# Kernel optimization log

Measured on AMD Instinct MI355X. Metric: run time of the kernel, lower is better.

Reference implementation:

```python
import jax, jax.numpy as jnp
import numpy as np
import math

C_S, C_Z = 384, 128
N_HEAD, C = 12, 16
N_QP, N_PV = 4, 8
B, N_RES = 1, 384


def quat_to_rot(q):
    # q: (..., 4) unnormalized quaternion -> (..., 3, 3) rotation matrix
    q = q / jnp.linalg.norm(q, axis=-1, keepdims=True)
    w, x, y, z = q[..., 0], q[..., 1], q[..., 2], q[..., 3]
    R = jnp.stack([
        1 - 2 * (y * y + z * z), 2 * (x * y - w * z), 2 * (x * z + w * y),
        2 * (x * y + w * z), 1 - 2 * (x * x + z * z), 2 * (y * z - w * x),
        2 * (x * z - w * y), 2 * (y * z + w * x), 1 - 2 * (x * x + y * y),
    ], axis=-1)
    return R.reshape(q.shape[:-1] + (3, 3))


def warp_3d_point(T, p):
    # T: (..., 1, 1, N, 4, 4) rigid transforms; p: (..., H, P, N, 3)
    R = T[..., :3, :3]
    t = T[..., :3, 3]
    return jnp.squeeze(R @ p[..., None], -1) + t


def warp_3d_point_inv(T, p):
    # Inverse rigid transform: R^T (p - t)
    R = T[..., :3, :3]
    t = T[..., :3, 3]
    return jnp.squeeze(jnp.swapaxes(R, -1, -2) @ (p - t)[..., None], -1)


def setup_inputs() -> dict:
    key = jax.random.key(0)
    ks = jax.random.split(key, 24)
    s = jax.random.normal(ks[0], (B, N_RES, C_S), dtype=jnp.float32)
    z = jax.random.normal(ks[1], (B, N_RES, N_RES, C_Z), dtype=jnp.float32)
    # Build rigid backbone transforms T (rotation from random quaternion + translation)
    quat = jax.random.normal(ks[2], (B, N_RES, 4), dtype=jnp.float32)
    trans = jax.random.normal(ks[3], (B, N_RES, 3), dtype=jnp.float32) * 10.0
    R = quat_to_rot(quat)
    T = jnp.zeros((B, N_RES, 4, 4), dtype=jnp.float32)
    T = T.at[..., :3, :3].set(R)
    T = T.at[..., :3, 3].set(trans)
    T = T.at[..., 3, 3].set(1.0)

    def lin(k, din, dout):
        kw, kb = jax.random.split(k)
        W = jax.random.normal(kw, (din, dout), dtype=jnp.float32) * 0.02
        b = jax.random.normal(kb, (dout,), dtype=jnp.float32) * 0.01
        return W, b

    Wq, bq = lin(ks[4], C_S, N_HEAD * C)
    Wk, bk = lin(ks[5], C_S, N_HEAD * C)
    Wv, bv = lin(ks[6], C_S, N_HEAD * C)
    Wqp, bqp = lin(ks[7], C_S, 3 * N_QP * N_HEAD)
    Wkp, bkp = lin(ks[8], C_S, 3 * N_QP * N_HEAD)
    Wvp, bvp = lin(ks[9], C_S, 3 * N_PV * N_HEAD)
    Wb, bb = lin(ks[10], C_Z, N_HEAD)
    d_out_in = N_HEAD * C_Z + N_HEAD * C + N_HEAD * 4 * N_PV
    Wo, bo = lin(ks[11], d_out_in, C_S)
    head_weights = jax.random.normal(ks[12], (N_HEAD,), dtype=jnp.float32) * 0.1
    return dict(s=s, z=z, T=T, Wq=Wq, bq=bq, Wk=Wk, bk=bk, Wv=Wv, bv=bv,
                Wqp=Wqp, bqp=bqp, Wkp=Wkp, bkp=bkp, Wvp=Wvp, bvp=bvp,
                Wb=Wb, bb=bb, Wo=Wo, bo=bo, head_weights=head_weights)


def ipa_forward(s, z, T, Wq, bq, Wk, bk, Wv, bv, Wqp, bqp, Wkp, bkp,
                Wvp, bvp, Wb, bb, Wo, bo, head_weights):
    batch = s.shape[:-2]
    n = s.shape[-2]
    # --- prepare qkv ---
    def heads(x):  # (..., N, H*C) -> (..., H, N, C)
        return jnp.moveaxis(x.reshape(batch + (n, N_HEAD, C)), -3, -2)
    q = heads(s @ Wq + bq)
    k = heads(s @ Wk + bk)
    v = heads(s @ Wv + bv)

    def pts(x, P):  # (..., N, 3*H*P) -> (..., H, P, N, 3)
        x = x.reshape(batch + (n, 3, N_HEAD, P))
        return jnp.moveaxis(x, (-4, -3), (-2, -1))
    qp = pts(s @ Wqp + bqp, N_QP)
    kp = pts(s @ Wkp + bkp, N_QP)
    vp = pts(s @ Wvp + bvp, N_PV)

    # --- attention scores (Alg 22 line 7) ---
    wc = math.sqrt(2.0 / (9.0 * N_QP))
    wl = math.sqrt(1.0 / 3.0)
    gamma = jax.nn.softplus(head_weights).reshape(-1, 1, 1)  # (H,1,1)
    q = q * (1.0 / math.sqrt(C))
    bias = jnp.moveaxis(z @ Wb + bb, -1, -3)  # (..., H, N, N)
    qk = jnp.einsum('...hic,...hjc->...hij', q, k)
    T_bc = T.reshape(batch + (1, 1, n, 4, 4))
    tqp = warp_3d_point(T_bc, qp)[..., :, None, :]   # (..., H, QP, N, 1, 3)
    tkp = warp_3d_point(T_bc, kp)[..., None, :, :]   # (..., H, QP, 1, N, 3)
    sq_dist = jnp.sum((tqp - tkp) ** 2, axis=-1)      # (..., H, QP, N, N)
    qpkp_term = gamma * (wc / 2.0) * jnp.sum(sq_dist, axis=-3)  # (..., H, N, N)
    att = jax.nn.softmax(wl * (qk + bias - qpkp_term), axis=-1)

    # --- outputs ---
    pairwise = jnp.einsum('...ijc,...hij->...hic', z, att)
    pairwise = jnp.moveaxis(pairwise, -3, -2).reshape(batch + (n, N_HEAD * C_Z))
    v_out = jnp.einsum('...hij,...hjc->...hic', att, v)
    v_out = jnp.moveaxis(v_out, -3, -2).reshape(batch + (n, N_HEAD * C))
    vt = warp_3d_point(T_bc, vp)                                # (..., H, PV, N, 3)
    v_att = jnp.einsum('...hij,...hkjp->...hkip', att, vt)     # (..., H, PV, N, 3)
    v_tr = warp_3d_point_inv(T_bc, v_att)                       # (..., H, PV, N, 3)
    v_tr = jnp.einsum('...hpic->...ichp', v_tr)                 # (..., N, 3, H, PV)
    norm = jnp.linalg.norm(v_tr, axis=-3, keepdims=True)        # (..., N, 1, H, PV)
    vp_norm = norm.reshape(batch + (n, N_HEAD * N_PV))
    vp_out = v_tr.reshape(batch + (n, 3 * N_HEAD * N_PV))

    out = jnp.concatenate([v_out, vp_out, vp_norm, pairwise], axis=-1)
    return out @ Wo + bo


def reference(s, z, T, Wq, bq, Wk, bk, Wv, bv, Wqp, bqp, Wkp, bkp,
              Wvp, bvp, Wb, bb, Wo, bo, head_weights):
    return ipa_forward(s, z, T, Wq, bq, Wk, bk, Wv, bv, Wqp, bqp, Wkp, bkp,
                       Wvp, bvp, Wb, bb, Wo, bo, head_weights)
```

## Files before the change

kernel.cpp:

```cpp
#include <hip/hip_runtime.h>
#include <math.h>

#define NRES 384
#define NH   12
#define WLc 0.5773502691896258f
#define WCc 0.23570226039551587f

typedef __attribute__((ext_vector_type(8))) _Float16 half8;
typedef __attribute__((ext_vector_type(4))) float f32x4;

#define OFF_P    0
#define OFF_PW   0
#define OFF_SH   442368
#define OFF_WCT  516096
#define OFF_BCT  737280
#define OFF_QE   738432
#define OFF_KE   885888
#define OFF_VET  1033344
#define OFF_WOT  1143936
#define OFF_CAT  1549440
#define OFF_ATT  1954944
#define OFF_BIAS 2839680
#define OFF_Z16  3724416

__global__ __launch_bounds__(256) void pack_bias(
    const float* __restrict__ s,  const float* __restrict__ z,
    const float* __restrict__ Wq,  const float* __restrict__ bq,
    const float* __restrict__ Wk,  const float* __restrict__ bk,
    const float* __restrict__ Wv,  const float* __restrict__ bv,
    const float* __restrict__ Wqp, const float* __restrict__ bqp,
    const float* __restrict__ Wkp, const float* __restrict__ bkp,
    const float* __restrict__ Wvp, const float* __restrict__ bvp,
    const float* __restrict__ Wb,  const float* __restrict__ bb,
    const float* __restrict__ Wo,
    float* __restrict__ ws)
{
    int b = blockIdx.x, t = threadIdx.x;
    __shared__ float tile[64 * 65];
    __shared__ _Float16 wbT[16 * 136];
    __shared__ float sbb[16];
    __shared__ _Float16 zL[64 * 136];

    if (b >= 451) {
        _Float16* biasb = (_Float16*)(ws + OFF_BIAS);
        _Float16* z16t  = (_Float16*)(ws + OFF_Z16);
        int bi = b - 451;
        size_t m0 = (size_t)bi * 64;
        int ib = bi / 6, j0 = (bi % 6) * 64;
        if (t < 128) {
            #pragma unroll
            for (int h = 0; h < 12; h++) wbT[h * 136 + t] = (_Float16)(WLc * Wb[t * 12 + h]);
            #pragma unroll
            for (int h = 12; h < 16; h++) wbT[h * 136 + t] = (_Float16)0.f;
        }
        if (t < 16) sbb[t] = (t < 12) ? WLc * bb[t] : 0.f;
        __syncthreads();
        int w = t >> 6, lane = t & 63;
        int m = lane & 15, q = lane >> 4;
        size_t ri = m0 + w * 16 + m;
        const float* zr = z + ri * 128 + q * 8;
        f32x4 acc = {0};
        #pragma unroll
        for (int sI = 0; sI < 4; sI++) {
            float4 v0 = *(const float4*)(zr + sI * 32);
            float4 v1 = *(const float4*)(zr + sI * 32 + 4);
            half8 a;
            a[0]=(_Float16)v0.x; a[1]=(_Float16)v0.y; a[2]=(_Float16)v0.z; a[3]=(_Float16)v0.w;
            a[4]=(_Float16)v1.x; a[5]=(_Float16)v1.y; a[6]=(_Float16)v1.z; a[7]=(_Float16)v1.w;
            *(half8*)(zL + (w * 16 + m) * 136 + sI * 32 + q * 8) = a;
            half8 bf = *(const half8*)(wbT + m * 136 + sI * 32 + q * 8);
            acc = __builtin_amdgcn_mfma_f32_16x16x32_f16(a, bf, acc, 0, 0, 0);
        }
        __syncthreads();
        {
            int c = t & 127, jh = t >> 7;
            _Float16 vals[32];
            #pragma unroll
            for (int u = 0; u < 32; u++) vals[u] = zL[(jh * 32 + u) * 136 + c];
            _Float16* dst = z16t + ((size_t)ib * 128 + c) * 384 + j0 + jh * 32;
            #pragma unroll
            for (int g = 0; g < 4; g++) {
                half8 r;
                #pragma unroll
                for (int u = 0; u < 8; u++) r[u] = vals[g * 8 + u];
                *(half8*)(dst + g * 8) = r;
            }
        }
        if (m < 12) {
            #pragma unroll
            for (int r = 0; r < 4; r++)
                biasb[(size_t)m * 147456 + m0 + w * 16 + q * 4 + r] = (_Float16)(acc[r] + sbb[m]);
        }
        return;
    }

    _Float16* sh  = (_Float16*)(ws + OFF_SH);
    _Float16* wct = (_Float16*)(ws + OFF_WCT);
    _Float16* wot = (_Float16*)(ws + OFF_WOT);
    float* bct = ws + OFF_BCT;

    if (b < 144) {
        int id = b * 256 + t;
        float4 v = ((const float4*)s)[id];
        _Float16 r[4] = { (_Float16)v.x, (_Float16)v.y, (_Float16)v.z, (_Float16)v.w };
        *(uint2*)(sh + id * 4) = *(uint2*)r;
        return;
    }
    if (b < 252) {
        int ti = b - 144;
        int k0 = (ti % 6) * 64, n0 = (ti / 6) * 64;
        int cl = t & 63, rg = t >> 6;
        int ncat = n0 + cl;
        const float* W; int dout, col;
        if      (ncat < 192) { W = Wq;  dout = 192; col = ncat; }
        else if (ncat < 384) { W = Wk;  dout = 192; col = ncat - 192; }
        else if (ncat < 576) { W = Wv;  dout = 192; col = ncat - 384; }
        else if (ncat < 720) { W = Wqp; dout = 144; col = ncat - 576; }
        else if (ncat < 864) { W = Wkp; dout = 144; col = ncat - 720; }
        else                 { W = Wvp; dout = 288; col = ncat - 864; }
        #pragma unroll
        for (int u = 0; u < 16; u++) {
            int r = rg * 16 + u;
            tile[r * 65 + cl] = W[(size_t)(k0 + r) * dout + col];
        }
        __syncthreads();
        #pragma unroll
        for (int u2 = 0; u2 < 2; u2++) {
            int item = t + 256 * u2;
            int nl = item >> 3, kg = item & 7;
            half8 rr;
            #pragma unroll
            for (int jj = 0; jj < 8; jj++) rr[jj] = (_Float16)tile[(kg * 8 + jj) * 65 + nl];
            *(half8*)(wct + (size_t)(n0 + nl) * 384 + k0 + kg * 8) = rr;
        }
        return;
    }
    if (b < 450) {
        int ti = b - 252;
        int k0 = (ti % 33) * 64, n0 = (ti / 33) * 64;
        int cl = t & 63, rg = t >> 6;
        #pragma unroll
        for (int u = 0; u < 16; u++) {
            int r = rg * 16 + u;
            tile[r * 65 + cl] = Wo[(size_t)(k0 + r) * 384 + n0 + cl];
        }
        __syncthreads();
        #pragma unroll
        for (int u2 = 0; u2 < 2; u2++) {
            int item = t + 256 * u2;
            int nl = item >> 3, kg = item & 7;
            half8 rr;
            #pragma unroll
            for (int jj = 0; jj < 8; jj++) rr[jj] = (_Float16)tile[(kg * 8 + jj) * 65 + nl];
            *(half8*)(wot + (size_t)(n0 + nl) * 2112 + k0 + kg * 8) = rr;
        }
        return;
    }
    for (int e = t; e < 1152; e += 256) {
        float bv_;
        if      (e < 192) bv_ = bq[e];
        else if (e < 384) bv_ = bk[e - 192];
        else if (e < 576) bv_ = bv[e - 384];
        else if (e < 720) bv_ = bqp[e - 576];
        else if (e < 864) bv_ = bkp[e - 720];
        else              bv_ = bvp[e - 864];
        bct[e] = bv_;
    }
}

__global__ __launch_bounds__(256) void proj_mfma(float* __restrict__ ws)
{
    const _Float16* sh  = (const _Float16*)(ws + OFF_SH);
    const _Float16* wct = (const _Float16*)(ws + OFF_WCT);
    const float* bct = ws + OFF_BCT;
    float* P = ws + OFF_P;

    __shared__ float sAcc[2][16][65];

    int t = threadIdx.x, w = t >> 6, lane = t & 63;
    int m = lane & 15, q = lane >> 4;
    int mh = w & 1, kh = w >> 1;
    int n0 = blockIdx.x * 64, m0 = blockIdx.y * 32 + mh * 16;

    f32x4 acc[4] = {0};
    const _Float16* arow = sh + (size_t)(m0 + m) * 384 + kh * 192;
    #pragma unroll 3
    for (int s = 0; s < 6; s++) {
        int k = s * 32 + q * 8;
        half8 a = *(const half8*)(arow + k);
        #pragma unroll
        for (int nt = 0; nt < 4; nt++) {
            half8 b = *(const half8*)(wct + (size_t)(n0 + nt * 16 + m) * 384 + kh * 192 + k);
            acc[nt] = __builtin_amdgcn_mfma_f32_16x16x32_f16(a, b, acc[nt], 0, 0, 0);
        }
    }
    if (kh == 0) {
        #pragma unroll
        for (int nt = 0; nt < 4; nt++)
            #pragma unroll
            for (int r = 0; r < 4; r++)
                sAcc[mh][q * 4 + r][nt * 16 + m] = acc[nt][r];
    }
    __syncthreads();
    if (kh == 1) {
        #pragma unroll
        for (int nt = 0; nt < 4; nt++) {
            int col = n0 + nt * 16 + m;
            float bias = bct[col];
            #pragma unroll
            for (int r = 0; r < 4; r++)
                P[(size_t)(m0 + q * 4 + r) * 1152 + col] =
                    acc[nt][r] + sAcc[mh][q * 4 + r][nt * 16 + m] + bias;
        }
    }
}

__global__ __launch_bounds__(192) void prep_kernel(
    const float* __restrict__ T, const float* __restrict__ hw,
    const float* __restrict__ bo, float* __restrict__ out,
    float* __restrict__ ws)
{
    int i = blockIdx.x, t = threadIdx.x;
    const float* pr = ws + OFF_P + (size_t)i * 1152;
    float* Qe = ws + OFF_QE;
    float* Ke = ws + OFF_KE;
    _Float16* vet = (_Float16*)(ws + OFF_VET);

    out[(size_t)i * 384 + t]       = bo[t];
    out[(size_t)i * 384 + 192 + t] = bo[192 + t];

    __shared__ float sT[16], sG[12];
    __shared__ float sTQ[12][4][3], sTK[12][4][3];
    if (t < 16) sT[t] = T[i * 16 + t];
    if (t < 12) { float x = hw[t]; sG[t] = (x > 20.f) ? x : log1pf(__expf(x)); }
    __syncthreads();
    float R00=sT[0],R01=sT[1],R02=sT[2],t0=sT[3];
    float R10=sT[4],R11=sT[5],R12=sT[6],t1=sT[7];
    float R20=sT[8],R21=sT[9],R22=sT[10],t2=sT[11];

    if (t < 48) {
        int h = t >> 2, p = t & 3;
        float a0 = pr[576 + 0*48 + h*4 + p], a1 = pr[576 + 1*48 + h*4 + p], a2 = pr[576 + 2*48 + h*4 + p];
        sTQ[h][p][0] = R00*a0 + R01*a1 + R02*a2 + t0;
        sTQ[h][p][1] = R10*a0 + R11*a1 + R12*a2 + t1;
        sTQ[h][p][2] = R20*a0 + R21*a1 + R22*a2 + t2;
    } else if (t < 96) {
        int tt = t - 48, h = tt >> 2, p = tt & 3;
        float a0 = pr[720 + 0*48 + h*4 + p], a1 = pr[720 + 1*48 + h*4 + p], a2 = pr[720 + 2*48 + h*4 + p];
        sTK[h][p][0] = R00*a0 + R01*a1 + R02*a2 + t0;
        sTK[h][p][1] = R10*a0 + R11*a1 + R12*a2 + t1;
        sTK[h][p][2] = R20*a0 + R21*a1 + R22*a2 + t2;
    } else {
        int tt = t - 96, h = tt >> 3, p = tt & 7;
        float a0 = pr[864 + 0*96 + h*8 + p], a1 = pr[864 + 1*96 + h*8 + p], a2 = pr[864 + 2*96 + h*8 + p];
        vet[(size_t)(h*48 + 16 + p*3 + 0) * 384 + i] = (_Float16)(R00*a0 + R01*a1 + R02*a2 + t0);
        vet[(size_t)(h*48 + 16 + p*3 + 1) * 384 + i] = (_Float16)(R10*a0 + R11*a1 + R12*a2 + t1);
        vet[(size_t)(h*48 + 16 + p*3 + 2) * 384 + i] = (_Float16)(R20*a0 + R21*a1 + R22*a2 + t2);
    }
    {
        int h = t >> 4, c = t & 15;
        vet[(size_t)(h*48 + c) * 384 + i] = (_Float16)pr[384 + h*16 + c];
        if (t < 96) vet[(size_t)((t>>3)*48 + 40 + (t&7)) * 384 + i] = (_Float16)0.f;
        Qe[(size_t)i*384 + h*32 + c] = WLc * 0.25f * pr[h*16 + c];
        Ke[((size_t)h*384 + i)*32 + c] = pr[192 + h*16 + c];
    }
    __syncthreads();
    if (t < 144) {
        int h = t / 12, d = t % 12, p = d / 3, r = d % 3;
        float gw = WLc * sG[h] * WCc;
        Qe[(size_t)i*384 + h*32 + 16 + d] = gw * sTQ[h][p][r];
        Ke[((size_t)h*384 + i)*32 + 16 + d] = sTK[h][p][r];
    }
    if (t < 12) {
        int h = t;
        float sqq = 0.f, sqk = 0.f;
        #pragma unroll
        for (int p = 0; p < 4; p++)
            #pragma unroll
            for (int r = 0; r < 3; r++) { sqq += sTQ[h][p][r]*sTQ[h][p][r]; sqk += sTK[h][p][r]*sTK[h][p][r]; }
        float gw = WLc * sG[h] * WCc;
        Qe[(size_t)i*384 + h*32 + 28] = -0.5f * gw;
        Qe[(size_t)i*384 + h*32 + 29] = -0.5f * gw * sqq;
        Qe[(size_t)i*384 + h*32 + 30] = 0.f;
        Qe[(size_t)i*384 + h*32 + 31] = 0.f;
        Ke[((size_t)h*384 + i)*32 + 28] = sqk;
        Ke[((size_t)h*384 + i)*32 + 29] = 1.f;
        Ke[((size_t)h*384 + i)*32 + 30] = 0.f;
        Ke[((size_t)h*384 + i)*32 + 31] = 0.f;
    }
}

__global__ __launch_bounds__(512) void logits_out40(
    const float* __restrict__ T, float* __restrict__ ws)
{
    __shared__ float sQe[8 * 32];
    __shared__ float sLg[8][384];
    __shared__ float sMS[16];
    __shared__ _Float16 sAttL[8 * 392];
    __shared__ float sO[8 * 49];
    __shared__ float sT8[8 * 16];

    int h = blockIdx.y, i0 = blockIdx.x * 8;
    int t = threadIdx.x;
    const float* Qe = ws + OFF_QE;
    const float* Ke = ws + OFF_KE;
    const _Float16* biasb = (const _Float16*)(ws + OFF_BIAS);
    const _Float16* vet = (const _Float16*)(ws + OFF_VET);
    _Float16* attg = (_Float16*)(ws + OFF_ATT);
    _Float16* catb = (_Float16*)(ws + OFF_CAT);

    {
        int bid = blockIdx.y * 48 + blockIdx.x;
        if (t < 256)
            ((float4*)(ws + OFF_PW))[bid * 256 + t] = (float4){0.f, 0.f, 0.f, 0.f};
    }
    if (t < 256)
        sQe[t] = Qe[(size_t)(i0 + (t >> 5)) * 384 + h * 32 + (t & 31)];
    if (t < 128)
        sT8[t] = T[(size_t)(i0 + (t >> 4)) * 16 + (t & 15)];
    __syncthreads();

    float lgv[8];
    if (t < 384) {
        int j = t;
        float ke[32];
        const float4* kr = (const float4*)(Ke + ((size_t)h * 384 + j) * 32);
        #pragma unroll
        for (int u = 0; u < 8; u++) { float4 v = kr[u]; ke[u*4]=v.x; ke[u*4+1]=v.y; ke[u*4+2]=v.z; ke[u*4+3]=v.w; }
        #pragma unroll
        for (int ii = 0; ii < 8; ii++) {
            float acc = (float)biasb[(size_t)h * 147456 + (size_t)(i0 + ii) * 384 + j];
            #pragma unroll
            for (int c = 0; c < 32; c++) acc += sQe[ii * 32 + c] * ke[c];
            lgv[ii] = acc;
            sLg[ii][j] = acc;
        }
    }
    __syncthreads();
    {
        int w = t >> 6, lane = t & 63;
        float vv[6], mx = -1e30f;
        #pragma unroll
        for (int u = 0; u < 6; u++) { vv[u] = sLg[w][lane + 64 * u]; mx = fmaxf(mx, vv[u]); }
        #pragma unroll
        for (int off = 1; off < 64; off <<= 1) mx = fmaxf(mx, __shfl_xor(mx, off));
        float sm = 0.f;
        #pragma unroll
        for (int u = 0; u < 6; u++) sm += __expf(vv[u] - mx);
        #pragma unroll
        for (int off = 1; off < 64; off <<= 1) sm += __shfl_xor(sm, off);
        if (lane == 0) { sMS[w] = mx; sMS[8 + w] = sm; }
    }
    __syncthreads();
    if (t < 384) {
        int j = t;
        #pragma unroll
        for (int ii = 0; ii < 8; ii++) {
            float a = __expf(lgv[ii] - sMS[ii]) * (1.0f / sMS[8 + ii]);
            attg[((size_t)h * 384 + i0 + ii) * 384 + j] = (_Float16)a;
            sAttL[ii * 392 + j] = (_Float16)a;
        }
    }
    __syncthreads();

    int w = t >> 6, lane = t & 63;
    int m16 = lane & 15, q = lane >> 4;
    if (w < 3) {
        int nt = w;
        f32x4 acc = {0};
        #pragma unroll 3
        for (int s = 0; s < 12; s++) {
            int k = s * 32 + q * 8;
            half8 a;
            if (m16 < 8) a = *(const half8*)(sAttL + m16 * 392 + k);
            else         a = (half8){0,0,0,0,0,0,0,0};
            half8 bfr = *(const half8*)(vet + (size_t)(h * 48 + nt * 16 + m16) * 384 + k);
            acc = __builtin_amdgcn_mfma_f32_16x16x32_f16(a, bfr, acc, 0, 0, 0);
        }
        #pragma unroll
        for (int r = 0; r < 4; r++) {
            int row = q * 4 + r;
            if (row < 8) sO[row * 49 + nt * 16 + m16] = acc[r];
        }
    }
    __syncthreads();

    if (t < 128) {
        int il = t >> 4, c = t & 15;
        catb[(size_t)(i0 + il) * 576 + h * 16 + c] = (_Float16)sO[il * 49 + c];
    }
    if (t < 64) {
        int il = t >> 3, p = t & 7;
        const float* o = sO + il * 49 + 16 + p * 3;
        const float* Ti = sT8 + il * 16;
        float x0 = o[0] - Ti[3], x1 = o[1] - Ti[7], x2 = o[2] - Ti[11];
        float r0 = Ti[0]*x0 + Ti[4]*x1 + Ti[8]*x2;
        float r1 = Ti[1]*x0 + Ti[5]*x1 + Ti[9]*x2;
        float r2 = Ti[2]*x0 + Ti[6]*x1 + Ti[10]*x2;
        _Float16* cr = catb + (size_t)(i0 + il) * 576;
        cr[192 + 0*96 + h*8 + p] = (_Float16)r0;
        cr[192 + 1*96 + h*8 + p] = (_Float16)r1;
        cr[192 + 2*96 + h*8 + p] = (_Float16)r2;
        cr[480 + h*8 + p] = (_Float16)sqrtf(r0*r0 + r1*r1 + r2*r2);
    }
}

__global__ __launch_bounds__(256) void pairwise_mfma(float* __restrict__ ws)
{
    int i = blockIdx.x, jc = blockIdx.y;
    int t = threadIdx.x, w = t >> 6, lane = t & 63;
    int m16 = lane & 15, q = lane >> 4;
    const _Float16* attg = (const _Float16*)(ws + OFF_ATT);
    const _Float16* z16t = (const _Float16*)(ws + OFF_Z16);
    float* PW = ws + OFF_PW;

    f32x4 acc0 = {0}, acc1 = {0};
    const _Float16* arow  = attg + ((size_t)(m16 < 12 ? m16 : 0) * 384 + i) * 384 + jc * 128;
    const _Float16* zrow0 = z16t + ((size_t)i * 128 + w * 32 + m16) * 384 + jc * 128;
    const _Float16* zrow1 = zrow0 + 16 * 384;
    #pragma unroll
    for (int ks = 0; ks < 4; ks++) {
        int k = ks * 32 + q * 8;
        half8 a;
        if (m16 < 12) a = *(const half8*)(arow + k);
        else          a = (half8){0,0,0,0,0,0,0,0};
        half8 b0 = *(const half8*)(zrow0 + k);
        half8 b1 = *(const half8*)(zrow1 + k);
        acc0 = __builtin_amdgcn_mfma_f32_16x16x32_f16(a, b0, acc0, 0, 0, 0);
        acc1 = __builtin_amdgcn_mfma_f32_16x16x32_f16(a, b1, acc1, 0, 0, 0);
    }
    if (q < 3) {
        #pragma unroll
        for (int r = 0; r < 4; r++) {
            int h = q * 4 + r;
            atomicAdd(&PW[(size_t)i * 1536 + h * 128 + w * 32 + m16],      acc0[r]);
            atomicAdd(&PW[(size_t)i * 1536 + h * 128 + w * 32 + 16 + m16], acc1[r]);
        }
    }
}

__global__ __launch_bounds__(256) void outgemm_mfma(
    float* __restrict__ ws, float* __restrict__ out)
{
    const _Float16* catb = (const _Float16*)(ws + OFF_CAT);
    const float* PW = ws + OFF_PW;
    const _Float16* wot = (const _Float16*)(ws + OFF_WOT);

    __shared__ float sAcc[2][16][65];

    int t = threadIdx.x, w = t >> 6, lane = t & 63;
    int m = lane & 15, q = lane >> 4;
    int mh = w & 1, kh = w >> 1;
    int n0 = blockIdx.x * 64;
    int m0 = blockIdx.y * 32 + mh * 16;
    int kbase = blockIdx.z * 704 + kh * 352;

    f32x4 acc[4] = {0};
    int row = m0 + m;
    #pragma unroll 2
    for (int s = 0; s < 11; s++) {
        int kb = kbase + s * 32;
        int k = kb + q * 8;
        half8 a;
        if (kb < 576) {
            a = *(const half8*)(catb + (size_t)row * 576 + k);
        } else {
            const float* pwp = PW + (size_t)row * 1536 + (k - 576);
            float4 u0 = ((const float4*)pwp)[0];
            float4 u1 = ((const float4*)pwp)[1];
            a[0]=(_Float16)u0.x; a[1]=(_Float16)u0.y; a[2]=(_Float16)u0.z; a[3]=(_Float16)u0.w;
            a[4]=(_Float16)u1.x; a[5]=(_Float16)u1.y; a[6]=(_Float16)u1.z; a[7]=(_Float16)u1.w;
        }
        #pragma unroll
        for (int nt = 0; nt < 4; nt++) {
            half8 b = *(const half8*)(wot + (size_t)(n0 + nt * 16 + m) * 2112 + k);
            acc[nt] = __builtin_amdgcn_mfma_f32_16x16x32_f16(a, b, acc[nt], 0, 0, 0);
        }
    }
    if (kh == 0) {
        #pragma unroll
        for (int nt = 0; nt < 4; nt++)
            #pragma unroll
            for (int r = 0; r < 4; r++)
                sAcc[mh][q * 4 + r][nt * 16 + m] = acc[nt][r];
    }
    __syncthreads();
    if (kh == 1) {
        #pragma unroll
        for (int nt = 0; nt < 4; nt++) {
            int col = n0 + nt * 16 + m;
            #pragma unroll
            for (int r = 0; r < 4; r++)
                atomicAdd(&out[(size_t)(m0 + q * 4 + r) * 384 + col],
                          acc[nt][r] + sAcc[mh][q * 4 + r][nt * 16 + m]);
        }
    }
}

extern "C" void kernel_launch(void* const* d_in, const int* in_sizes, int n_in,
                              void* d_out, int out_size, void* d_ws, size_t ws_size,
                              hipStream_t stream)
{
    const float* s   = (const float*)d_in[0];
    const float* z   = (const float*)d_in[1];
    const float* T   = (const float*)d_in[2];
    const float* Wq  = (const float*)d_in[3];
    const float* bq  = (const float*)d_in[4];
    const float* Wk  = (const float*)d_in[5];
    const float* bk  = (const float*)d_in[6];
    const float* Wv  = (const float*)d_in[7];
    const float* bv  = (const float*)d_in[8];
    const float* Wqp = (const float*)d_in[9];
    const float* bqp = (const float*)d_in[10];
    const float* Wkp = (const float*)d_in[11];
    const float* bkp = (const float*)d_in[12];
    const float* Wvp = (const float*)d_in[13];
    const float* bvp = (const float*)d_in[14];
    const float* Wb  = (const float*)d_in[15];
    const float* bb  = (const float*)d_in[16];
    const float* Wo  = (const float*)d_in[17];
    const float* bo  = (const float*)d_in[18];
    const float* hw  = (const float*)d_in[19];
    float* ws  = (float*)d_ws;
    float* out = (float*)d_out;

    pack_bias<<<2755, 256, 0, stream>>>(s, z, Wq, bq, Wk, bk, Wv, bv,
                                        Wqp, bqp, Wkp, bkp, Wvp, bvp, Wb, bb, Wo, ws);
    proj_mfma<<<dim3(18, 12), 256, 0, stream>>>(ws);
    prep_kernel<<<384, 192, 0, stream>>>(T, hw, bo, out, ws);
    logits_out40<<<dim3(48, 12), 512, 0, stream>>>(T, ws);
    pairwise_mfma<<<dim3(384, 3), 256, 0, stream>>>(ws);
    outgemm_mfma<<<dim3(6, 12, 3), 256, 0, stream>>>(ws, out);
}
```

Measured before the change: 216.8 us.

## Fuse all IPA stages into one persistent cooperative kernel with grid syncs

Replaces the six separate kernel launches with a single cooperative persistent kernel that loops over each stage's work items and separates stages with grid-wide barriers. The aim is to remove per-launch overhead and the idle tail between dependent kernels. The old launch sequence stays as a fallback if the cooperative launch fails. In exchange, the logits stage now runs with 256 threads instead of 512. Grid syncs across up to 2048 blocks have their own cost, and shared memory is a single union buffer sized for the largest stage.

```diff
diff --git a/kernel.cpp b/kernel.cpp
--- a/kernel.cpp
+++ b/kernel.cpp
@@ -1,5 +1,8 @@
 #include <hip/hip_runtime.h>
+#include <hip/hip_cooperative_groups.h>
 #include <math.h>
+
+namespace cg = cooperative_groups;
 
 #define NRES 384
 #define NH   12
@@ -22,6 +25,489 @@
 #define OFF_ATT  1954944
 #define OFF_BIAS 2839680
 #define OFF_Z16  3724416
+
+__global__ __launch_bounds__(256, 3) void mega_ipa(
+    const float* __restrict__ s,  const float* __restrict__ z,
+    const float* __restrict__ T,  const float* __restrict__ hw,
+    const float* __restrict__ Wq,  const float* __restrict__ bq,
+    const float* __restrict__ Wk,  const float* __restrict__ bk,
+    const float* __restrict__ Wv,  const float* __restrict__ bv,
+    const float* __restrict__ Wqp, const float* __restrict__ bqp,
+    const float* __restrict__ Wkp, const float* __restrict__ bkp,
+    const float* __restrict__ Wvp, const float* __restrict__ bvp,
+    const float* __restrict__ Wb,  const float* __restrict__ bb,
+    const float* __restrict__ Wo,  const float* __restrict__ bo,
+    float* __restrict__ ws, float* __restrict__ out)
+{
+    cg::grid_group grid = cg::this_grid();
+    __shared__ __attribute__((aligned(16))) char smem[21888];
+
+    const int t = threadIdx.x;
+    const int bid = blockIdx.x;
+    const int G = gridDim.x;
+    const int w = t >> 6, lane = t & 63;
+    const int m16 = lane & 15, q4 = lane >> 4;
+
+    {
+        float* tile    = (float*)smem;
+        _Float16* zL   = (_Float16*)smem;
+        _Float16* wbT  = (_Float16*)(smem + 17408);
+        float* sbb     = (float*)(smem + 21760);
+        _Float16* sh   = (_Float16*)(ws + OFF_SH);
+        _Float16* wct  = (_Float16*)(ws + OFF_WCT);
+        _Float16* wot  = (_Float16*)(ws + OFF_WOT);
+        float* bct     = ws + OFF_BCT;
+        _Float16* biasb = (_Float16*)(ws + OFF_BIAS);
+        _Float16* z16t  = (_Float16*)(ws + OFF_Z16);
+
+        for (int b = bid; b < 2755; b += G) {
+            if (b >= 451) {
+                int bi = b - 451;
+                size_t m0 = (size_t)bi * 64;
+                int ib = bi / 6, j0 = (bi % 6) * 64;
+                if (t < 128) {
+                    #pragma unroll
+                    for (int h = 0; h < 12; h++) wbT[h * 136 + t] = (_Float16)(WLc * Wb[t * 12 + h]);
+                    #pragma unroll
+                    for (int h = 12; h < 16; h++) wbT[h * 136 + t] = (_Float16)0.f;
+                }
+                if (t < 16) sbb[t] = (t < 12) ? WLc * bb[t] : 0.f;
+                __syncthreads();
+                size_t ri = m0 + w * 16 + m16;
+                const float* zr = z + ri * 128 + q4 * 8;
+                f32x4 acc = {0};
+                #pragma unroll
+                for (int sI = 0; sI < 4; sI++) {
+                    float4 v0 = *(const float4*)(zr + sI * 32);
+                    float4 v1 = *(const float4*)(zr + sI * 32 + 4);
+                    half8 a;
+                    a[0]=(_Float16)v0.x; a[1]=(_Float16)v0.y; a[2]=(_Float16)v0.z; a[3]=(_Float16)v0.w;
+                    a[4]=(_Float16)v1.x; a[5]=(_Float16)v1.y; a[6]=(_Float16)v1.z; a[7]=(_Float16)v1.w;
+                    *(half8*)(zL + (w * 16 + m16) * 136 + sI * 32 + q4 * 8) = a;
+                    half8 bf = *(const half8*)(wbT + m16 * 136 + sI * 32 + q4 * 8);
+                    acc = __builtin_amdgcn_mfma_f32_16x16x32_f16(a, bf, acc, 0, 0, 0);
+                }
+                __syncthreads();
+                {
+                    int c = t & 127, jh = t >> 7;
+                    _Float16 vals[32];
+                    #pragma unroll
+                    for (int u = 0; u < 32; u++) vals[u] = zL[(jh * 32 + u) * 136 + c];
+                    _Float16* dst = z16t + ((size_t)ib * 128 + c) * 384 + j0 + jh * 32;
+                    #pragma unroll
+                    for (int g = 0; g < 4; g++) {
+                        half8 r;
+                        #pragma unroll
+                        for (int u = 0; u < 8; u++) r[u] = vals[g * 8 + u];
+                        *(half8*)(dst + g * 8) = r;
+                    }
+                }
+                if (m16 < 12) {
+                    #pragma unroll
+                    for (int r = 0; r < 4; r++)
+                        biasb[(size_t)m16 * 147456 + m0 + w * 16 + q4 * 4 + r] = (_Float16)(acc[r] + sbb[m16]);
+                }
+            } else if (b < 144) {
+                int id = b * 256 + t;
+                float4 v = ((const float4*)s)[id];
+                _Float16 r[4] = { (_Float16)v.x, (_Float16)v.y, (_Float16)v.z, (_Float16)v.w };
+                *(uint2*)(sh + id * 4) = *(uint2*)r;
+            } else if (b < 252) {
+                int ti = b - 144;
+                int k0 = (ti % 6) * 64, n0 = (ti / 6) * 64;
+                int cl = t & 63, rg = t >> 6;
+                int ncat = n0 + cl;
+                const float* W; int dout, col;
+                if      (ncat < 192) { W = Wq;  dout = 192; col = ncat; }
+                else if (ncat < 384) { W = Wk;  dout = 192; col = ncat - 192; }
+                else if (ncat < 576) { W = Wv;  dout = 192; col = ncat - 384; }
+                else if (ncat < 720) { W = Wqp; dout = 144; col = ncat - 576; }
+                else if (ncat < 864) { W = Wkp; dout = 144; col = ncat - 720; }
+                else                 { W = Wvp; dout = 288; col = ncat - 864; }
+                #pragma unroll
+                for (int u = 0; u < 16; u++) {
+                    int r = rg * 16 + u;
+                    tile[r * 65 + cl] = W[(size_t)(k0 + r) * dout + col];
+                }
+                __syncthreads();
+                #pragma unroll
+                for (int u2 = 0; u2 < 2; u2++) {
+                    int item = t + 256 * u2;
+                    int nl = item >> 3, kg = item & 7;
+                    half8 rr;
+                    #pragma unroll
+                    for (int jj = 0; jj < 8; jj++) rr[jj] = (_Float16)tile[(kg * 8 + jj) * 65 + nl];
+                    *(half8*)(wct + (size_t)(n0 + nl) * 384 + k0 + kg * 8) = rr;
+                }
+            } else if (b < 450) {
+                int ti = b - 252;
+                int k0 = (ti % 33) * 64, n0 = (ti / 33) * 64;
+                int cl = t & 63, rg = t >> 6;
+                #pragma unroll
+                for (int u = 0; u < 16; u++) {
+                    int r = rg * 16 + u;
+                    tile[r * 65 + cl] = Wo[(size_t)(k0 + r) * 384 + n0 + cl];
+                }
+                __syncthreads();
+                #pragma unroll
+                for (int u2 = 0; u2 < 2; u2++) {
+                    int item = t + 256 * u2;
+                    int nl = item >> 3, kg = item & 7;
+                    half8 rr;
+                    #pragma unroll
+                    for (int jj = 0; jj < 8; jj++) rr[jj] = (_Float16)tile[(kg * 8 + jj) * 65 + nl];
+                    *(half8*)(wot + (size_t)(n0 + nl) * 2112 + k0 + kg * 8) = rr;
+                }
+            } else {
+                for (int e = t; e < 1152; e += 256) {
+                    float bv_;
+                    if      (e < 192) bv_ = bq[e];
+                    else if (e < 384) bv_ = bk[e - 192];
+                    else if (e < 576) bv_ = bv[e - 384];
+                    else if (e < 720) bv_ = bqp[e - 576];
+                    else if (e < 864) bv_ = bkp[e - 720];
+                    else              bv_ = bvp[e - 864];
+                    bct[e] = bv_;
+                }
+            }
+            __syncthreads();
+        }
+    }
+    grid.sync();
+
+    {
+        const _Float16* sh  = (const _Float16*)(ws + OFF_SH);
+        const _Float16* wct = (const _Float16*)(ws + OFF_WCT);
+        const float* bct = ws + OFF_BCT;
+        float* P = ws + OFF_P;
+        float* sAcc = (float*)smem;
+        int mh = w & 1, kh = w >> 1;
+
+        for (int b = bid; b < 216; b += G) {
+            int n0 = (b % 18) * 64, m0 = (b / 18) * 32 + mh * 16;
+            f32x4 acc[4] = {0};
+            const _Float16* arow = sh + (size_t)(m0 + m16) * 384 + kh * 192;
+            #pragma unroll 3
+            for (int ss = 0; ss < 6; ss++) {
+                int k = ss * 32 + q4 * 8;
+                half8 a = *(const half8*)(arow + k);
+                #pragma unroll
+                for (int nt = 0; nt < 4; nt++) {
+                    half8 bfr = *(const half8*)(wct + (size_t)(n0 + nt * 16 + m16) * 384 + kh * 192 + k);
+                    acc[nt] = __builtin_amdgcn_mfma_f32_16x16x32_f16(a, bfr, acc[nt], 0, 0, 0);
+                }
+            }
+            if (kh == 0) {
+                #pragma unroll
+                for (int nt = 0; nt < 4; nt++)
+                    #pragma unroll
+                    for (int r = 0; r < 4; r++)
+                        sAcc[(mh * 16 + q4 * 4 + r) * 65 + nt * 16 + m16] = acc[nt][r];
+            }
+            __syncthreads();
+            if (kh == 1) {
+                #pragma unroll
+                for (int nt = 0; nt < 4; nt++) {
+                    int col = n0 + nt * 16 + m16;
+                    float bias = bct[col];
+                    #pragma unroll
+                    for (int r = 0; r < 4; r++)
+                        P[(size_t)(m0 + q4 * 4 + r) * 1152 + col] =
+                            acc[nt][r] + sAcc[(mh * 16 + q4 * 4 + r) * 65 + nt * 16 + m16] + bias;
+                }
+            }
+            __syncthreads();
+        }
+    }
+    grid.sync();
+
+    {
+        float* sT  = (float*)smem;
+        float* sG  = (float*)(smem + 64);
+        float* sTQ = (float*)(smem + 128);
+        float* sTK = (float*)(smem + 704);
+        float* Qe = ws + OFF_QE;
+        float* Ke = ws + OFF_KE;
+        _Float16* vet = (_Float16*)(ws + OFF_VET);
+
+        for (int b = bid; b < 384; b += G) {
+            int i = b;
+            const float* pr = ws + OFF_P + (size_t)i * 1152;
+            if (t < 192) {
+                out[(size_t)i * 384 + t]       = bo[t];
+                out[(size_t)i * 384 + 192 + t] = bo[192 + t];
+            }
+            if (t < 16) sT[t] = T[i * 16 + t];
+            if (t < 12) { float x = hw[t]; sG[t] = (x > 20.f) ? x : log1pf(__expf(x)); }
+            __syncthreads();
+            float R00=sT[0],R01=sT[1],R02=sT[2],t0=sT[3];
+            float R10=sT[4],R11=sT[5],R12=sT[6],t1=sT[7];
+            float R20=sT[8],R21=sT[9],R22=sT[10],t2=sT[11];
+
+            if (t < 48) {
+                int h = t >> 2, p = t & 3;
+                float a0 = pr[576 + 0*48 + h*4 + p], a1 = pr[576 + 1*48 + h*4 + p], a2 = pr[576 + 2*48 + h*4 + p];
+                sTQ[(h*4+p)*3+0] = R00*a0 + R01*a1 + R02*a2 + t0;
+                sTQ[(h*4+p)*3+1] = R10*a0 + R11*a1 + R12*a2 + t1;
+                sTQ[(h*4+p)*3+2] = R20*a0 + R21*a1 + R22*a2 + t2;
+            } else if (t < 96) {
+                int tt = t - 48, h = tt >> 2, p = tt & 3;
+                float a0 = pr[720 + 0*48 + h*4 + p], a1 = pr[720 + 1*48 + h*4 + p], a2 = pr[720 + 2*48 + h*4 + p];
+                sTK[(h*4+p)*3+0] = R00*a0 + R01*a1 + R02*a2 + t0;
+                sTK[(h*4+p)*3+1] = R10*a0 + R11*a1 + R12*a2 + t1;
+                sTK[(h*4+p)*3+2] = R20*a0 + R21*a1 + R22*a2 + t2;
+            } else if (t < 192) {
+                int tt = t - 96, h = tt >> 3, p = tt & 7;
+                float a0 = pr[864 + 0*96 + h*8 + p], a1 = pr[864 + 1*96 + h*8 + p], a2 = pr[864 + 2*96 + h*8 + p];
+                vet[(size_t)(h*48 + 16 + p*3 + 0) * 384 + i] = (_Float16)(R00*a0 + R01*a1 + R02*a2 + t0);
+                vet[(size_t)(h*48 + 16 + p*3 + 1) * 384 + i] = (_Float16)(R10*a0 + R11*a1 + R12*a2 + t1);
+                vet[(size_t)(h*48 + 16 + p*3 + 2) * 384 + i] = (_Float16)(R20*a0 + R21*a1 + R22*a2 + t2);
+            }
+            if (t < 192) {
+                int h = t >> 4, c = t & 15;
+                vet[(size_t)(h*48 + c) * 384 + i] = (_Float16)pr[384 + h*16 + c];
+                if (t < 96) vet[(size_t)((t>>3)*48 + 40 + (t&7)) * 384 + i] = (_Float16)0.f;
+                Qe[(size_t)i*384 + h*32 + c] = WLc * 0.25f * pr[h*16 + c];
+                Ke[((size_t)h*384 + i)*32 + c] = pr[192 + h*16 + c];
+            }
+            __syncthreads();
+            if (t < 144) {
+                int h = t / 12, d = t % 12, p = d / 3, r = d % 3;
+                float gw = WLc * sG[h] * WCc;
+                Qe[(size_t)i*384 + h*32 + 16 + d] = gw * sTQ[(h*4+p)*3+r];
+                Ke[((size_t)h*384 + i)*32 + 16 + d] = sTK[(h*4+p)*3+r];
+            }
+            if (t < 12) {
+                int h = t;
+                float sqq = 0.f, sqk = 0.f;
+                #pragma unroll
+                for (int p = 0; p < 4; p++)
+                    #pragma unroll
+                    for (int r = 0; r < 3; r++) {
+                        sqq += sTQ[(h*4+p)*3+r]*sTQ[(h*4+p)*3+r];
+                        sqk += sTK[(h*4+p)*3+r]*sTK[(h*4+p)*3+r];
+                    }
+                float gw = WLc * sG[h] * WCc;
+                Qe[(size_t)i*384 + h*32 + 28] = -0.5f * gw;
+                Qe[(size_t)i*384 + h*32 + 29] = -0.5f * gw * sqq;
+                Qe[(size_t)i*384 + h*32 + 30] = 0.f;
+                Qe[(size_t)i*384 + h*32 + 31] = 0.f;
+                Ke[((size_t)h*384 + i)*32 + 28] = sqk;
+                Ke[((size_t)h*384 + i)*32 + 29] = 1.f;
+                Ke[((size_t)h*384 + i)*32 + 30] = 0.f;
+                Ke[((size_t)h*384 + i)*32 + 31] = 0.f;
+            }
+            __syncthreads();
+        }
+    }
+    grid.sync();
+
+    {
+        float* sQe = (float*)smem;
+        float* sLg = (float*)(smem + 1024);
+        float* sMS = (float*)(smem + 13312);
+        _Float16* sAttL = (_Float16*)(smem + 13376);
+        float* sO  = (float*)(smem + 19648);
+        float* sT8 = (float*)(smem + 21216);
+        const float* Qe = ws + OFF_QE;
+        const float* Ke = ws + OFF_KE;
+        const _Float16* biasb = (const _Float16*)(ws + OFF_BIAS);
+        const _Float16* vet = (const _Float16*)(ws + OFF_VET);
+        _Float16* attg = (_Float16*)(ws + OFF_ATT);
+        _Float16* catb = (_Float16*)(ws + OFF_CAT);
+
+        for (int b = bid; b < 576; b += G) {
+            int h = b / 48, i0 = (b % 48) * 8;
+            ((float4*)(ws + OFF_PW))[b * 256 + t] = (float4){0.f, 0.f, 0.f, 0.f};
+            sQe[t] = Qe[(size_t)(i0 + (t >> 5)) * 384 + h * 32 + (t & 31)];
+            if (t < 128) sT8[t] = T[(size_t)(i0 + (t >> 4)) * 16 + (t & 15)];
+            __syncthreads();
+
+            float lgv[2][8];
+            if (t < 192) {
+                #pragma unroll
+                for (int jj = 0; jj < 2; jj++) {
+                    int j = t + jj * 192;
+                    float ke[32];
+                    const float4* kr = (const float4*)(Ke + ((size_t)h * 384 + j) * 32);
+                    #pragma unroll
+                    for (int u = 0; u < 8; u++) {
+                        float4 v = kr[u];
+                        ke[u*4]=v.x; ke[u*4+1]=v.y; ke[u*4+2]=v.z; ke[u*4+3]=v.w;
+                    }
+                    #pragma unroll
+                    for (int ii = 0; ii < 8; ii++) {
+                        float acc = (float)biasb[(size_t)h * 147456 + (size_t)(i0 + ii) * 384 + j];
+                        #pragma unroll
+                        for (int c = 0; c < 32; c++) acc += sQe[ii * 32 + c] * ke[c];
+                        lgv[jj][ii] = acc;
+                        sLg[ii * 384 + j] = acc;
+                    }
+                }
+            }
+            __syncthreads();
+            {
+                #pragma unroll
+                for (int rr = 0; rr < 2; rr++) {
+                    int row = w * 2 + rr;
+                    float vv[6], mx = -1e30f;
+                    #pragma unroll
+                    for (int u = 0; u < 6; u++) { vv[u] = sLg[row * 384 + lane + 64 * u]; mx = fmaxf(mx, vv[u]); }
+                    #pragma unroll
+                    for (int off = 1; off < 64; off <<= 1) mx = fmaxf(mx, __shfl_xor(mx, off));
+                    float sm = 0.f;
+                    #pragma unroll
+                    for (int u = 0; u < 6; u++) sm += __expf(vv[u] - mx);
+                    #pragma unroll
+                    for (int off = 1; off < 64; off <<= 1) sm += __shfl_xor(sm, off);
+                    if (lane == 0) { sMS[row] = mx; sMS[8 + row] = sm; }
+                }
+            }
+            __syncthreads();
+            if (t < 192) {
+                #pragma unroll
+                for (int jj = 0; jj < 2; jj++) {
+                    int j = t + jj * 192;
+                    #pragma unroll
+                    for (int ii = 0; ii < 8; ii++) {
+                        float a = __expf(lgv[jj][ii] - sMS[ii]) * (1.0f / sMS[8 + ii]);
+                        attg[((size_t)h * 384 + i0 + ii) * 384 + j] = (_Float16)a;
+                        sAttL[ii * 392 + j] = (_Float16)a;
+                    }
+                }
+            }
+            __syncthreads();
+            if (w < 3) {
+                int nt = w;
+                f32x4 acc = {0};
+                #pragma unroll 3
+                for (int ss = 0; ss < 12; ss++) {
+                    int k = ss * 32 + q4 * 8;
+                    half8 a;
+                    if (m16 < 8) a = *(const half8*)(sAttL + m16 * 392 + k);
+                    else         a = (half8){0,0,0,0,0,0,0,0};
+                    half8 bfr = *(const half8*)(vet + (size_t)(h * 48 + nt * 16 + m16) * 384 + k);
+                    acc = __builtin_amdgcn_mfma_f32_16x16x32_f16(a, bfr, acc, 0, 0, 0);
+                }
+                #pragma unroll
+                for (int r = 0; r < 4; r++) {
+                    int row = q4 * 4 + r;
+                    if (row < 8) sO[row * 49 + nt * 16 + m16] = acc[r];
+                }
+            }
+            __syncthreads();
+            if (t < 128) {
+                int il = t >> 4, c = t & 15;
+                catb[(size_t)(i0 + il) * 576 + h * 16 + c] = (_Float16)sO[il * 49 + c];
+            }
+            if (t < 64) {
+                int il = t >> 3, p = t & 7;
+                const float* o = sO + il * 49 + 16 + p * 3;
+                const float* Ti = sT8 + il * 16;
+                float x0 = o[0] - Ti[3], x1 = o[1] - Ti[7], x2 = o[2] - Ti[11];
+                float r0 = Ti[0]*x0 + Ti[4]*x1 + Ti[8]*x2;
+                float r1 = Ti[1]*x0 + Ti[5]*x1 + Ti[9]*x2;
+                float r2 = Ti[2]*x0 + Ti[6]*x1 + Ti[10]*x2;
+                _Float16* cr = catb + (size_t)(i0 + il) * 576;
+                cr[192 + 0*96 + h*8 + p] = (_Float16)r0;
+                cr[192 + 1*96 + h*8 + p] = (_Float16)r1;
+                cr[192 + 2*96 + h*8 + p] = (_Float16)r2;
+                cr[480 + h*8 + p] = (_Float16)sqrtf(r0*r0 + r1*r1 + r2*r2);
+            }
+            __syncthreads();
+        }
+    }
+    grid.sync();
+
+    {
+        const _Float16* attg = (const _Float16*)(ws + OFF_ATT);
+        const _Float16* z16t = (const _Float16*)(ws + OFF_Z16);
+        float* PW = ws + OFF_PW;
+
+        for (int b = bid; b < 1152; b += G) {
+            int i = b % 384, jc = b / 384;
+            f32x4 acc0 = {0}, acc1 = {0};
+            const _Float16* arow  = attg + ((size_t)(m16 < 12 ? m16 : 0) * 384 + i) * 384 + jc * 128;
+            const _Float16* zrow0 = z16t + ((size_t)i * 128 + w * 32 + m16) * 384 + jc * 128;
+            const _Float16* zrow1 = zrow0 + 16 * 384;
+            #pragma unroll
+            for (int ks = 0; ks < 4; ks++) {
+                int k = ks * 32 + q4 * 8;
+                half8 a;
+                if (m16 < 12) a = *(const half8*)(arow + k);
+                else          a = (half8){0,0,0,0,0,0,0,0};
+                half8 b0 = *(const half8*)(zrow0 + k);
+                half8 b1 = *(const half8*)(zrow1 + k);
+                acc0 = __builtin_amdgcn_mfma_f32_16x16x32_f16(a, b0, acc0, 0, 0, 0);
+                acc1 = __builtin_amdgcn_mfma_f32_16x16x32_f16(a, b1, acc1, 0, 0, 0);
+            }
+            if (q4 < 3) {
+                #pragma unroll
+                for (int r = 0; r < 4; r++) {
+                    int h = q4 * 4 + r;
+                    atomicAdd(&PW[(size_t)i * 1536 + h * 128 + w * 32 + m16],      acc0[r]);
+                    atomicAdd(&PW[(size_t)i * 1536 + h * 128 + w * 32 + 16 + m16], acc1[r]);
+                }
+            }
+        }
+    }
+    grid.sync();
+
+    {
+        const _Float16* catb = (const _Float16*)(ws + OFF_CAT);
+        const float* PW = ws + OFF_PW;
+        const _Float16* wot = (const _Float16*)(ws + OFF_WOT);
+        float* sAcc = (float*)smem;
+        int mh = w & 1, kh = w >> 1;
+
+        for (int b = bid; b < 216; b += G) {
+            int n0 = (b % 6) * 64;
+            int m0 = ((b / 6) % 12) * 32 + mh * 16;
+            int kbase = (b / 72) * 704 + kh * 352;
+            f32x4 acc[4] = {0};
+            int row = m0 + m16;
+            #pragma unroll 2
+            for (int ss = 0; ss < 11; ss++) {
+                int kb = kbase + ss * 32;
+                int k = kb + q4 * 8;
+                half8 a;
+                if (kb < 576) {
+                    a = *(const half8*)(catb + (size_t)row * 576 + k);
+                } else {
+                    const float* pwp = PW + (size_t)row * 1536 + (k - 576);
+                    float4 u0 = ((const float4*)pwp)[0];
+                    float4 u1 = ((const float4*)pwp)[1];
+                    a[0]=(_Float16)u0.x; a[1]=(_Float16)u0.y; a[2]=(_Float16)u0.z; a[3]=(_Float16)u0.w;
+                    a[4]=(_Float16)u1.x; a[5]=(_Float16)u1.y; a[6]=(_Float16)u1.z; a[7]=(_Float16)u1.w;
+                }
+                #pragma unroll
+                for (int nt = 0; nt < 4; nt++) {
+                    half8 bfr = *(const half8*)(wot + (size_t)(n0 + nt * 16 + m16) * 2112 + k);
+                    acc[nt] = __builtin_amdgcn_mfma_f32_16x16x32_f16(a, bfr, acc[nt], 0, 0, 0);
+                }
+            }
+            if (kh == 0) {
+                #pragma unroll
+                for (int nt = 0; nt < 4; nt++)
+                    #pragma unroll
+                    for (int r = 0; r < 4; r++)
+                        sAcc[(mh * 16 + q4 * 4 + r) * 65 + nt * 16 + m16] = acc[nt][r];
+            }
+            __syncthreads();
+            if (kh == 1) {
+                #pragma unroll
+                for (int nt = 0; nt < 4; nt++) {
+                    int col = n0 + nt * 16 + m16;
+                    #pragma unroll
+                    for (int r = 0; r < 4; r++)
+                        atomicAdd(&out[(size_t)(m0 + q4 * 4 + r) * 384 + col],
+                                  acc[nt][r] + sAcc[(mh * 16 + q4 * 4 + r) * 65 + nt * 16 + m16]);
+                }
+            }
+            __syncthreads();
+        }
+    }
+}
 
 __global__ __launch_bounds__(256) void pack_bias(
     const float* __restrict__ s,  const float* __restrict__ z,
@@ -174,14 +660,11 @@
     const _Float16* wct = (const _Float16*)(ws + OFF_WCT);
     const float* bct = ws + OFF_BCT;
     float* P = ws + OFF_P;
-
     __shared__ float sAcc[2][16][65];
-
     int t = threadIdx.x, w = t >> 6, lane = t & 63;
     int m = lane & 15, q = lane >> 4;
     int mh = w & 1, kh = w >> 1;
     int n0 = blockIdx.x * 64, m0 = blockIdx.y * 32 + mh * 16;
-
     f32x4 acc[4] = {0};
     const _Float16* arow = sh + (size_t)(m0 + m) * 384 + kh * 192;
     #pragma unroll 3
@@ -445,16 +928,13 @@
     const _Float16* catb = (const _Float16*)(ws + OFF_CAT);
     const float* PW = ws + OFF_PW;
     const _Float16* wot = (const _Float16*)(ws + OFF_WOT);
-
     __shared__ float sAcc[2][16][65];
-
     int t = threadIdx.x, w = t >> 6, lane = t & 63;
     int m = lane & 15, q = lane >> 4;
     int mh = w & 1, kh = w >> 1;
     int n0 = blockIdx.x * 64;
     int m0 = blockIdx.y * 32 + mh * 16;
     int kbase = blockIdx.z * 704 + kh * 352;
-
     f32x4 acc[4] = {0};
     int row = m0 + m;
     #pragma unroll 2
@@ -524,11 +1004,30 @@
     float* ws  = (float*)d_ws;
     float* out = (float*)d_out;
 
-    pack_bias<<<2755, 256, 0, stream>>>(s, z, Wq, bq, Wk, bk, Wv, bv,
-                                        Wqp, bqp, Wkp, bkp, Wvp, bvp, Wb, bb, Wo, ws);
-    proj_mfma<<<dim3(18, 12), 256, 0, stream>>>(ws);
-    prep_kernel<<<384, 192, 0, stream>>>(T, hw, bo, out, ws);
-    logits_out40<<<dim3(48, 12), 512, 0, stream>>>(T, ws);
-    pairwise_mfma<<<dim3(384, 3), 256, 0, stream>>>(ws);
-    outgemm_mfma<<<dim3(6, 12, 3), 256, 0, stream>>>(ws, out);
+    int nb = 0;
+    hipError_t qerr = hipOccupancyMaxActiveBlocksPerMultiprocessor(&nb, mega_ipa, 256, 0);
+    hipError_t lerr = hipErrorUnknown;
+    if (qerr == hipSuccess && nb > 0) {
+        int gridx = nb * 256;
+        if (gridx > 2048) gridx = 2048;
+        void* args[] = {
+            (void*)&s, (void*)&z, (void*)&T, (void*)&hw,
+            (void*)&Wq, (void*)&bq, (void*)&Wk, (void*)&bk,
+            (void*)&Wv, (void*)&bv, (void*)&Wqp, (void*)&bqp,
+            (void*)&Wkp, (void*)&bkp, (void*)&Wvp, (void*)&bvp,
+            (void*)&Wb, (void*)&bb, (void*)&Wo, (void*)&bo,
+            (void*)&ws, (void*)&out
+        };
+        lerr = hipLaunchCooperativeKernel(mega_ipa, dim3(gridx), dim3(256),
+                                          args, 0u, stream);
+    }
+    if (lerr != hipSuccess) {
+        pack_bias<<<2755, 256, 0, stream>>>(s, z, Wq, bq, Wk, bk, Wv, bv,
+                                            Wqp, bqp, Wkp, bkp, Wvp, bvp, Wb, bb, Wo, ws);
+        proj_mfma<<<dim3(18, 12), 256, 0, stream>>>(ws);
+        prep_kernel<<<384, 192, 0, stream>>>(T, hw, bo, out, ws);
+        logits_out40<<<dim3(48, 12), 512, 0, stream>>>(T, ws);
+        pairwise_mfma<<<dim3(384, 3), 256, 0, stream>>>(ws);
+        outgemm_mfma<<<dim3(6, 12, 3), 256, 0, stream>>>(ws, out);
+    }
 }
```

Result: slower. 431.0 us (+98.8%).
